# Performance work log

Hardware: AMD Instinct MI355X
Metric: run time of the kernel (lower is better)

The kernel has to match this reference:

```python
import jax, jax.numpy as jnp
import numpy as np
import math

N = 50_000       # points (CSR segments)
V = 500_000      # mapped views (ragged rows)
IN_MAIN, IN_MAP, IN_MOD = 64, 16, 128
NC, NC_QK = 32, 8
EPS = 1e-12


def setup_inputs() -> dict:
    key = jax.random.key(0)
    ks = jax.random.split(key, 18)
    def rn(k, shape, fan_in=None):
        s = (1.0 / math.sqrt(fan_in)) if fan_in else 1.0
        return jax.random.normal(k, shape, jnp.float32) * s
    x_main = rn(ks[0], (N, IN_MAIN))
    x_mod = rn(ks[1], (V, IN_MOD))
    x_map = rn(ks[2], (V, IN_MAP))
    # CSR pointers: monotone, csr[0]=0, csr[-1]=V (full row coverage)
    inner = jnp.sort(jax.random.randint(ks[3], (N - 1,), 0, V))
    csr_idx = jnp.concatenate([jnp.zeros(1, jnp.int32), inner.astype(jnp.int32),
                               jnp.full((1,), V, jnp.int32)])
    return {
        "x_main": x_main, "x_mod": x_mod, "x_map": x_map, "csr_idx": csr_idx,
        # E_main: MLP([in_main, nc, nc], bias=False)
        "W_main1": rn(ks[4], (IN_MAIN, NC), IN_MAIN),
        "W_main2": rn(ks[5], (NC, NC), NC),
        # E_map (DeepSetFeat): elementwise MLP + segment-max set context + fuse
        "W_map1": rn(ks[6], (IN_MAP, NC), IN_MAP),
        "W_map2": rn(ks[7], (2 * NC, NC), 2 * NC),
        # E_mod: MLP([in_mod, in_mod, in_mod], bias=False)
        "W_mod1": rn(ks[8], (IN_MOD, IN_MOD), IN_MOD),
        "W_mod2": rn(ks[9], (IN_MOD, IN_MOD), IN_MOD),
        # Q, K linear heads (nc_inner -> nc_qk * num_groups), with bias
        "WQ": rn(ks[10], (NC, NC_QK), NC), "bQ": jnp.zeros((NC_QK,), jnp.float32),
        "WK": rn(ks[11], (NC, NC_QK), NC), "bK": jnp.zeros((NC_QK,), jnp.float32),
        # Gating(num_groups=1): weight init ones, bias init zeros
        "g_w": jnp.ones((1, 1), jnp.float32), "g_b": jnp.zeros((1, 1), jnp.float32),
    }


def reference(x_main, x_mod, x_map, csr_idx,
              W_main1, W_main2, W_map1, W_map2, W_mod1, W_mod2,
              WQ, bQ, WK, bK, g_w, g_b):
    counts = csr_idx[1:] - csr_idx[:-1]                     # [N]
    dense_idx = jnp.repeat(jnp.arange(N, dtype=jnp.int32), counts,
                           total_repeat_length=V)           # [V]
    nonempty = counts > 0                                   # [N]

    # --- encoders ---
    h_main = jax.nn.relu(x_main @ W_main1) @ W_main2        # [N, NC]
    h = jax.nn.relu(x_map @ W_map1)                         # [V, NC]
    set_ctx = jax.ops.segment_max(h, dense_idx, num_segments=N)
    set_ctx = jnp.where(nonempty[:, None], set_ctx, 0.0)    # empty segs -> 0
    h_map = jax.nn.relu(jnp.concatenate([h, set_ctx[dense_idx]], axis=1) @ W_map2)  # [V, NC]
    h_mod = jax.nn.relu(x_mod @ W_mod1) @ W_mod2            # [V, IN_MOD]

    # --- Q/K compatibilities (num_groups=1) ---
    keys = h_map @ WK + bK                                  # [V, NC_QK]
    queries = (h_main @ WQ + bQ)[dense_idx]                 # [V, NC_QK]
    comp = jnp.sum(keys * queries, axis=1) / jnp.sqrt(jnp.float32(NC_QK))  # [V]

    # --- segment_softmax_csr ---
    seg_max = jax.ops.segment_max(comp, dense_idx, num_segments=N)
    seg_max = jnp.where(nonempty, seg_max, 0.0)
    cexp = jnp.exp(comp - seg_max[dense_idx])               # [V]
    seg_sum = jax.ops.segment_sum(cexp, dense_idx, num_segments=N) + EPS
    att = cexp / seg_sum[dense_idx]                         # [V]

    # --- attention-weighted pooling ---
    x_pool = jax.ops.segment_sum(h_mod * att[:, None], dense_idx, num_segments=N)  # [N, IN_MOD]

    # --- gating on per-segment max compatibility ---
    gate_in = jnp.where(nonempty, seg_max, 0.0)[:, None]    # [N, 1]
    gate = jnp.tanh(jax.nn.relu(g_w * gate_in + g_b))       # [N, 1]
    x_pool = x_pool * gate

    x_seen = nonempty
    return x_pool, x_seen
```

## Files before the change

### kernel.cpp

```cpp
#include <hip/hip_runtime.h>
#include <math.h>

#define N_PTS 50000
#define V_VIEWS 500000
#define IN_MAIN 64
#define IN_MAP 16
#define IN_MOD 128
#define NC 32
#define NC_QK 8
#define SEG_EPS 1e-12f

typedef short bf16x8 __attribute__((ext_vector_type(8)));
typedef float f32x4 __attribute__((ext_vector_type(4)));

static __device__ __forceinline__ short f2bf(float x) {
    union { float f; unsigned u; } v; v.f = x;
    unsigned r = v.u + 0x7fffu + ((v.u >> 16) & 1u);
    return (short)(r >> 16);
}


__global__ __launch_bounds__(256) void k0_setup(const int* __restrict__ csr,
                                                const float* __restrict__ Wmod1,
                                                const float* __restrict__ Wmod2,
                                                const float* __restrict__ Wm1,
                                                const float* __restrict__ Wm2,
                                                int* __restrict__ didx,
                                                float* __restrict__ pooled,
                                                float* __restrict__ ctxw,
                                                short* __restrict__ Wf,
                                                short* __restrict__ W1f,
                                                short* __restrict__ W2af,
                                                short* __restrict__ W2f) {
    int t = blockIdx.x * blockDim.x + threadIdx.x;
    int total = gridDim.x * blockDim.x;
    if (t < N_PTS) {
        int a = csr[t], b = csr[t + 1];
        for (int v = a; v < b; ++v) didx[v] = t;
    }
    for (int i = t; i < N_PTS * IN_MOD; i += total) pooled[i] = 0.f;
    for (int i = t; i < N_PTS * NC; i += total) ctxw[i] = 0.f;
    for (int i = t; i < IN_MOD * IN_MOD; i += total) {
        int e = i & 7, l = (i >> 3) & 63, j = (i >> 9) & 7, kk = i >> 12;
        int k = kk * 32 + ((l >> 4) << 3) + e;
        int ch = (j << 4) + (l & 15);
        Wf[i] = f2bf(Wmod1[k * IN_MOD + ch]);
        W2f[i] = f2bf(Wmod2[k * IN_MOD + ch]);
    }
    for (int i = t; i < 1024; i += total) {
        int e = i & 7, l = (i >> 3) & 63, j = i >> 9;
        int k = ((l >> 4) << 3) + e;
        int ch = (j << 4) + (l & 15);
        W1f[i] = (k < IN_MAP) ? f2bf(Wm1[k * NC + ch]) : (short)0;
        W2af[i] = f2bf(Wm2[k * NC + ch]);
    }
}

__global__ __launch_bounds__(256) void kA_main_q(
    const float* __restrict__ x_main, const float* __restrict__ W1,
    const float* __restrict__ W2, const float* __restrict__ WQ,
    const float* __restrict__ bQ, const float* __restrict__ WK,
    const float* __restrict__ bK,
    float* __restrict__ wq, float* __restrict__ qb) {
    __shared__ float W1l[IN_MAIN * NC];
    __shared__ float W2l[NC * NC];
    __shared__ float WQl[NC * NC_QK];
    __shared__ float WKl[NC * NC_QK];
    __shared__ float bQl[NC_QK];
    __shared__ float bKl[NC_QK];
    __shared__ float h1buf[8][NC];
    __shared__ float h2buf[8][NC];
    __shared__ float qbuf[8][NC_QK];
    int tid = threadIdx.x;
    for (int i = tid; i < IN_MAIN * NC; i += 256) W1l[i] = W1[i];
    for (int i = tid; i < NC * NC; i += 256) W2l[i] = W2[i];
    for (int i = tid; i < NC * NC_QK; i += 256) WQl[i] = WQ[i];
    for (int i = tid; i < NC * NC_QK; i += 256) WKl[i] = WK[i];
    if (tid < NC_QK) { bQl[tid] = bQ[tid]; bKl[tid] = bK[tid]; }
    __syncthreads();
    int g = tid >> 5, c = tid & 31;
    int p = blockIdx.x * 8 + g;
    float h1 = 0.f;
    if (p < N_PTS) {
        const float* xr = x_main + (size_t)p * IN_MAIN;
        for (int k = 0; k < IN_MAIN; ++k) h1 += xr[k] * W1l[k * NC + c];
        h1 = fmaxf(h1, 0.f);
    }
    h1buf[g][c] = h1;
    __syncthreads();
    float h2 = 0.f;
    for (int j = 0; j < NC; ++j) h2 += h1buf[g][j] * W2l[j * NC + c];
    h2buf[g][c] = h2;
    __syncthreads();
    if (c < NC_QK) {
        float acc = bQl[c];
        for (int j = 0; j < NC; ++j) acc += h2buf[g][j] * WQl[j * NC_QK + c];
        qbuf[g][c] = acc;
    }
    __syncthreads();
    if (p < N_PTS) {
        float w = 0.f;
        for (int j = 0; j < NC_QK; ++j) w += WKl[c * NC_QK + j] * qbuf[g][j];
        wq[(size_t)p * NC + c] = w;
        if (c == 0) {
            float b = 0.f;
            for (int j = 0; j < NC_QK; ++j) b += bKl[j] * qbuf[g][j];
            qb[p] = b;
        }
    }
}

__global__ __launch_bounds__(256) void kH_ctx(
    const float* __restrict__ x_map, const int* __restrict__ didx,
    const short* __restrict__ W1f, int* __restrict__ ctxbits) {
    int tid = threadIdx.x;
    int w = tid >> 6, lane = tid & 63;
    int vbase = blockIdx.x * 64 + w * 16;
    if (vbase >= V_VIEWS) return;
    const bf16x8* pW1 = (const bf16x8*)W1f;
    bf16x8 b1a = pW1[lane], b1b = pW1[64 + lane];

    bf16x8 a1 = (bf16x8){0, 0, 0, 0, 0, 0, 0, 0};
    if (lane < 32) {
        const float* xp = x_map + (size_t)(vbase + (lane & 15)) * IN_MAP + ((lane >> 4) << 3);
        float4 x0 = *(const float4*)xp;
        float4 x1 = *(const float4*)(xp + 4);
        a1[0] = f2bf(x0.x); a1[1] = f2bf(x0.y); a1[2] = f2bf(x0.z); a1[3] = f2bf(x0.w);
        a1[4] = f2bf(x1.x); a1[5] = f2bf(x1.y); a1[6] = f2bf(x1.z); a1[7] = f2bf(x1.w);
    }
    f32x4 d1a = (f32x4){0.f, 0.f, 0.f, 0.f}, d1b = (f32x4){0.f, 0.f, 0.f, 0.f};
    d1a = __builtin_amdgcn_mfma_f32_16x16x32_bf16(a1, b1a, d1a, 0, 0, 0);
    d1b = __builtin_amdgcn_mfma_f32_16x16x32_bf16(a1, b1b, d1b, 0, 0, 0);

    int c = lane & 15, kq = lane >> 4;
    int vg = vbase + (kq << 2);
    int4 ss = *(const int4*)(didx + vg);
    const int* sp = (const int*)&ss;
    float ma = 0.f, mb = 0.f;
#pragma unroll
    for (int r = 0; r < 4; ++r) {
        ma = fmaxf(ma, fmaxf(d1a[r], 0.f));
        mb = fmaxf(mb, fmaxf(d1b[r], 0.f));
        bool runend = (r == 3) || (sp[r + 1] != sp[r]);
        if (runend) {
            atomicMax(&ctxbits[sp[r] * NC + c], __float_as_int(ma));
            atomicMax(&ctxbits[sp[r] * NC + c + 16], __float_as_int(mb));
            ma = 0.f; mb = 0.f;
        }
    }
}

__global__ __launch_bounds__(256) void kB2b_ctxw(
    const float* __restrict__ Wm2, float* __restrict__ ctxw) {
    __shared__ float W2bl[NC * NC];
    __shared__ float ctxl[8][NC];
    int tid = threadIdx.x;
    for (int i = tid; i < NC * NC; i += 256) W2bl[i] = Wm2[NC * NC + i];
    int g = tid >> 5, c = tid & 31;
    int s = blockIdx.x * 8 + g;
    float cv = (s < N_PTS) ? ctxw[(size_t)s * NC + c] : 0.f;
    ctxl[g][c] = cv;
    __syncthreads();
    if (s < N_PTS) {
        float val = 0.f;
        for (int j = 0; j < NC; ++j) val += ctxl[g][j] * W2bl[j * NC + c];
        ctxw[(size_t)s * NC + c] = val;
    }
}

__global__ __launch_bounds__(256) void kB3_comp(
    const float* __restrict__ x_map, const int* __restrict__ didx,
    const short* __restrict__ W1f, const short* __restrict__ W2af,
    const float* __restrict__ ctxW2b, const float* __restrict__ wq,
    const float* __restrict__ qb, float* __restrict__ comp) {
    __shared__ float hl[4][16 * 36];
    int tid = threadIdx.x;
    int w = tid >> 6, lane = tid & 63;
    int vbase = blockIdx.x * 64 + w * 16;
    if (vbase >= V_VIEWS) return;
    const bf16x8* pW1 = (const bf16x8*)W1f;
    const bf16x8* pW2 = (const bf16x8*)W2af;
    bf16x8 b1a = pW1[lane], b1b = pW1[64 + lane];
    bf16x8 b2a = pW2[lane], b2b = pW2[64 + lane];

    bf16x8 a1 = (bf16x8){0, 0, 0, 0, 0, 0, 0, 0};
    if (lane < 32) {
        const float* xp = x_map + (size_t)(vbase + (lane & 15)) * IN_MAP + ((lane >> 4) << 3);
        float4 x0 = *(const float4*)xp;
        float4 x1 = *(const float4*)(xp + 4);
        a1[0] = f2bf(x0.x); a1[1] = f2bf(x0.y); a1[2] = f2bf(x0.z); a1[3] = f2bf(x0.w);
        a1[4] = f2bf(x1.x); a1[5] = f2bf(x1.y); a1[6] = f2bf(x1.z); a1[7] = f2bf(x1.w);
    }
    f32x4 d1a = (f32x4){0.f, 0.f, 0.f, 0.f}, d1b = (f32x4){0.f, 0.f, 0.f, 0.f};
    d1a = __builtin_amdgcn_mfma_f32_16x16x32_bf16(a1, b1a, d1a, 0, 0, 0);
    d1b = __builtin_amdgcn_mfma_f32_16x16x32_bf16(a1, b1b, d1b, 0, 0, 0);

    float* hw = hl[w];
    int c = lane & 15;
    int vr0 = (lane >> 4) << 2;
#pragma unroll
    for (int r = 0; r < 4; ++r) {
        hw[(vr0 + r) * 36 + c] = fmaxf(d1a[r], 0.f);
        hw[(vr0 + r) * 36 + c + 16] = fmaxf(d1b[r], 0.f);
    }
    const float* hr = hw + (lane & 15) * 36 + ((lane >> 4) << 3);
    float4 h0 = *(const float4*)hr;
    float4 h1 = *(const float4*)(hr + 4);
    bf16x8 a2;
    a2[0] = f2bf(h0.x); a2[1] = f2bf(h0.y); a2[2] = f2bf(h0.z); a2[3] = f2bf(h0.w);
    a2[4] = f2bf(h1.x); a2[5] = f2bf(h1.y); a2[6] = f2bf(h1.z); a2[7] = f2bf(h1.w);

    f32x4 d2a = (f32x4){0.f, 0.f, 0.f, 0.f}, d2b = (f32x4){0.f, 0.f, 0.f, 0.f};
    d2a = __builtin_amdgcn_mfma_f32_16x16x32_bf16(a2, b2a, d2a, 0, 0, 0);
    d2b = __builtin_amdgcn_mfma_f32_16x16x32_bf16(a2, b2b, d2b, 0, 0, 0);

    int vg = vbase + vr0;
    int4 ss = *(const int4*)(didx + vg);
    const int* sp = (const int*)&ss;
    float part[4];
#pragma unroll
    for (int r = 0; r < 4; ++r) {
        size_t so = (size_t)sp[r] * NC;
        float m0 = fmaxf(d2a[r] + ctxW2b[so + c], 0.f);
        float m1 = fmaxf(d2b[r] + ctxW2b[so + c + 16], 0.f);
        part[r] = m0 * wq[so + c] + m1 * wq[so + c + 16];
    }
#pragma unroll
    for (int mask = 1; mask < 16; mask <<= 1) {
#pragma unroll
        for (int r = 0; r < 4; ++r) part[r] += __shfl_xor(part[r], mask);
    }
    if (c == 0) {
        const float inv_sqrt = 0.35355339059327373f;
        float4 o;
        o.x = (part[0] + qb[sp[0]]) * inv_sqrt;
        o.y = (part[1] + qb[sp[1]]) * inv_sqrt;
        o.z = (part[2] + qb[sp[2]]) * inv_sqrt;
        o.w = (part[3] + qb[sp[3]]) * inv_sqrt;
        *(float4*)(comp + vg) = o;
    }
}

__global__ __launch_bounds__(256) void kB4_att(
    float* __restrict__ comp, const int* __restrict__ csr,
    float* __restrict__ segmax) {
    int wid = threadIdx.x >> 6, lane = threadIdx.x & 63;
    int seg = blockIdx.x * 4 + wid;
    if (seg >= N_PTS) return;
    int v0 = csr[seg], v1 = csr[seg + 1];
    if (v0 >= v1) {
        if (lane == 0) segmax[seg] = 0.f;
        return;
    }
    float mx = -__builtin_inff();
    for (int v = v0 + lane; v < v1; v += 64) mx = fmaxf(mx, comp[v]);
    for (int o = 32; o > 0; o >>= 1) mx = fmaxf(mx, __shfl_xor(mx, o));
    float sm = 0.f;
    for (int v = v0 + lane; v < v1; v += 64) sm += __expf(comp[v] - mx);
    for (int o = 32; o > 0; o >>= 1) sm += __shfl_xor(sm, o);
    float inv = 1.f / (sm + SEG_EPS);
    for (int v = v0 + lane; v < v1; v += 64) comp[v] = __expf(comp[v] - mx) * inv;
    if (lane == 0) segmax[seg] = mx;
}

#define VB 64
__global__ __launch_bounds__(256) void kC_pool(
    const float* __restrict__ x_mod, const short* __restrict__ Wf,
    const int* __restrict__ didx, const int* __restrict__ csr,
    const float* __restrict__ att, float* __restrict__ pooled) {
    __shared__ float Yl[VB * 132];
    __shared__ float attl[VB];
    __shared__ int didxl[VB];
    int tid = threadIdx.x;
    int vbase = blockIdx.x * VB;
    if (tid < VB) {
        int v = vbase + tid;
        if (v < V_VIEWS) {
            didxl[tid] = didx[v];
            attl[tid] = att[v];
        } else {
            didxl[tid] = didx[V_VIEWS - 1];
            attl[tid] = 0.f;
        }
    }
    __syncthreads();

    int w = tid >> 6, lane = tid & 63;
    int row16 = lane & 15;
    int kq = lane >> 4;
    int k0 = kq << 3;
    f32x4 acc[8];
    for (int j = 0; j < 8; ++j) acc[j] = (f32x4){0.f, 0.f, 0.f, 0.f};

    int v = vbase + w * 16 + row16;
    if (v >= V_VIEWS) v = V_VIEWS - 1;
    const float* xp = x_mod + (size_t)v * IN_MOD;

#pragma unroll
    for (int kk = 0; kk < 4; ++kk) {
        float4 x0 = *(const float4*)(xp + kk * 32 + k0);
        float4 x1 = *(const float4*)(xp + kk * 32 + k0 + 4);
        bf16x8 a;
        a[0] = f2bf(x0.x); a[1] = f2bf(x0.y); a[2] = f2bf(x0.z); a[3] = f2bf(x0.w);
        a[4] = f2bf(x1.x); a[5] = f2bf(x1.y); a[6] = f2bf(x1.z); a[7] = f2bf(x1.w);
        const bf16x8* wf = (const bf16x8*)(Wf + ((size_t)(kk * 8) * 64 + lane) * 8);
#pragma unroll
        for (int j = 0; j < 8; ++j) {
            bf16x8 b = wf[j * 64];
            acc[j] = __builtin_amdgcn_mfma_f32_16x16x32_bf16(a, b, acc[j], 0, 0, 0);
        }
    }
#pragma unroll
    for (int j = 0; j < 8; ++j) {
        int ch = j * 16 + row16;
        int rbase = w * 16 + (kq << 2);
#pragma unroll
        for (int r = 0; r < 4; ++r) {
            int rw = rbase + r;
            Yl[rw * 132 + ch] = fmaxf(acc[j][r], 0.f) * attl[rw];
        }
    }
    __syncthreads();
    if (tid < IN_MOD) {
        int c = tid;
        float s_acc = 0.f;
        int cur = didxl[0];
        for (int r = 0; r < VB; ++r) {
            int s = didxl[r];
            if (s != cur) {
                if (csr[cur] >= vbase && csr[cur + 1] <= vbase + VB)
                    pooled[(size_t)cur * IN_MOD + c] = s_acc;
                else
                    atomicAdd(&pooled[(size_t)cur * IN_MOD + c], s_acc);
                s_acc = 0.f; cur = s;
            }
            s_acc += Yl[r * 132 + c];
        }
        if (csr[cur] >= vbase && csr[cur + 1] <= vbase + VB)
            pooled[(size_t)cur * IN_MOD + c] = s_acc;
        else
            atomicAdd(&pooled[(size_t)cur * IN_MOD + c], s_acc);
    }
}

__global__ __launch_bounds__(256) void kD_final(
    const short* __restrict__ W2f,
    const float* __restrict__ segmax, const int* __restrict__ csr,
    const float* __restrict__ g_w, const float* __restrict__ g_b,
    float* __restrict__ out) {
    int tid = threadIdx.x;
    int w = tid >> 6, lane = tid & 63;
    int row16 = lane & 15;
    int kq = lane >> 4;
    int k0 = kq << 3;
    int rbase = blockIdx.x * 64 + w * 16;
    float gw = g_w[0], gb = g_b[0];

    int rr = rbase + row16;
    if (rr >= N_PTS) rr = N_PTS - 1;
    const float* xp = out + (size_t)rr * IN_MOD;

    f32x4 acc[8];
    for (int j = 0; j < 8; ++j) acc[j] = (f32x4){0.f, 0.f, 0.f, 0.f};
#pragma unroll
    for (int kk = 0; kk < 4; ++kk) {
        float4 x0 = *(const float4*)(xp + kk * 32 + k0);
        float4 x1 = *(const float4*)(xp + kk * 32 + k0 + 4);
        bf16x8 a;
        a[0] = f2bf(x0.x); a[1] = f2bf(x0.y); a[2] = f2bf(x0.z); a[3] = f2bf(x0.w);
        a[4] = f2bf(x1.x); a[5] = f2bf(x1.y); a[6] = f2bf(x1.z); a[7] = f2bf(x1.w);
        const bf16x8* wf = (const bf16x8*)(W2f + ((size_t)(kk * 8) * 64 + lane) * 8);
#pragma unroll
        for (int j = 0; j < 8; ++j) {
            bf16x8 b = wf[j * 64];
            acc[j] = __builtin_amdgcn_mfma_f32_16x16x32_bf16(a, b, acc[j], 0, 0, 0);
        }
    }
    float gate[4];
    int rowv[4];
#pragma unroll
    for (int r = 0; r < 4; ++r) {
        int ro = rbase + (kq << 2) + r;
        rowv[r] = ro;
        if (ro < N_PTS) {
            bool nz = csr[ro + 1] > csr[ro];
            float gin = nz ? segmax[ro] : 0.f;
            gate[r] = tanhf(fmaxf(gw * gin + gb, 0.f));
            if (row16 == 0) out[(size_t)N_PTS * IN_MOD + ro] = nz ? 1.f : 0.f;
        } else {
            gate[r] = 0.f;
        }
    }
#pragma unroll
    for (int j = 0; j < 8; ++j) {
        int ch = j * 16 + row16;
#pragma unroll
        for (int r = 0; r < 4; ++r) {
            if (rowv[r] < N_PTS)
                out[(size_t)rowv[r] * IN_MOD + ch] = acc[j][r] * gate[r];
        }
    }
}

extern "C" void kernel_launch(void* const* d_in, const int* in_sizes, int n_in,
                              void* d_out, int out_size, void* d_ws, size_t ws_size,
                              hipStream_t stream) {
    (void)in_sizes; (void)n_in; (void)out_size; (void)ws_size;
    const float* x_main = (const float*)d_in[0];
    const float* x_mod  = (const float*)d_in[1];
    const float* x_map  = (const float*)d_in[2];
    const int*   csr    = (const int*)d_in[3];
    const float* W_main1 = (const float*)d_in[4];
    const float* W_main2 = (const float*)d_in[5];
    const float* W_map1  = (const float*)d_in[6];
    const float* W_map2  = (const float*)d_in[7];
    const float* W_mod1  = (const float*)d_in[8];
    const float* W_mod2  = (const float*)d_in[9];
    const float* WQ = (const float*)d_in[10];
    const float* bQ = (const float*)d_in[11];
    const float* WK = (const float*)d_in[12];
    const float* bK = (const float*)d_in[13];
    const float* g_w = (const float*)d_in[14];
    const float* g_b = (const float*)d_in[15];
    float* out = (float*)d_out;

    char* ws = (char*)d_ws;
    int*   didx   = (int*)ws;
    float* wq     = (float*)(ws + 2000000);
    float* qb     = (float*)(ws + 8400000);
    float* ctxw   = (float*)(ws + 8600000);
    float* comp   = (float*)(ws + 15000000);
    float* segmax = (float*)(ws + 17000000);
    short* Wf     = (short*)(ws + 17200000);
    short* W1f    = (short*)(ws + 17240000);
    short* W2af   = (short*)(ws + 17244000);
    short* W2f    = (short*)(ws + 17248000);
    float* pooled = out;

    k0_setup<<<512, 256, 0, stream>>>(csr, W_mod1, W_mod2, W_map1, W_map2,
                                      didx, pooled, ctxw, Wf, W1f, W2af, W2f);
    kA_main_q<<<(N_PTS + 7) / 8, 256, 0, stream>>>(x_main, W_main1, W_main2, WQ, bQ,
                                                   WK, bK, wq, qb);
    kH_ctx<<<(V_VIEWS + 63) / 64, 256, 0, stream>>>(x_map, didx, W1f, (int*)ctxw);
    kB2b_ctxw<<<(N_PTS + 7) / 8, 256, 0, stream>>>(W_map2, ctxw);
    kB3_comp<<<(V_VIEWS + 63) / 64, 256, 0, stream>>>(x_map, didx, W1f, W2af,
                                                      ctxw, wq, qb, comp);
    kB4_att<<<(N_PTS + 3) / 4, 256, 0, stream>>>(comp, csr, segmax);
    kC_pool<<<(V_VIEWS + VB - 1) / VB, 256, 0, stream>>>(x_mod, Wf, didx, csr,
                                                         comp, pooled);
    kD_final<<<(N_PTS + 63) / 64, 256, 0, stream>>>(W2f, segmax, csr, g_w, g_b, out);
}
```

Measured before the change: 235.0 us.

## Cache bf16 map hidden layer, defer softmax normalization, split pooling scan

kH_ctx now writes the first-layer map activations as bf16 to a workspace buffer, so kB3_comp loads them instead of rereading x_map and recomputing the first MFMA. kB4_att no longer rewrites comp with normalized attention. It stores a per-segment inverse sum, and kC_pool computes exp(comp - max) * invsum on the fly. The pooling segment scan in kC_pool is split across 256 threads as two 32-row halves instead of 128 threads over 64 rows, which may raise atomic traffic at the half boundary. The cost is an extra 32 MB bf16 write and read for hbuf in exchange for less recompute and one fewer full pass over comp.

```diff
diff --git a/kernel.cpp b/kernel.cpp
--- a/kernel.cpp
+++ b/kernel.cpp
@@ -112,7 +112,9 @@
 
 __global__ __launch_bounds__(256) void kH_ctx(
     const float* __restrict__ x_map, const int* __restrict__ didx,
-    const short* __restrict__ W1f, int* __restrict__ ctxbits) {
+    const short* __restrict__ W1f, int* __restrict__ ctxbits,
+    short* __restrict__ hbuf) {
+    __shared__ float hl[4][16 * 36];
     int tid = threadIdx.x;
     int w = tid >> 6, lane = tid & 63;
     int vbase = blockIdx.x * 64 + w * 16;
@@ -133,7 +135,22 @@
     d1b = __builtin_amdgcn_mfma_f32_16x16x32_bf16(a1, b1b, d1b, 0, 0, 0);
 
     int c = lane & 15, kq = lane >> 4;
-    int vg = vbase + (kq << 2);
+    int vr0 = kq << 2;
+    float* hw = hl[w];
+#pragma unroll
+    for (int r = 0; r < 4; ++r) {
+        hw[(vr0 + r) * 36 + c] = fmaxf(d1a[r], 0.f);
+        hw[(vr0 + r) * 36 + c + 16] = fmaxf(d1b[r], 0.f);
+    }
+    const float* hr = hw + c * 36 + (kq << 3);
+    float4 h0 = *(const float4*)hr;
+    float4 h1 = *(const float4*)(hr + 4);
+    bf16x8 a2;
+    a2[0] = f2bf(h0.x); a2[1] = f2bf(h0.y); a2[2] = f2bf(h0.z); a2[3] = f2bf(h0.w);
+    a2[4] = f2bf(h1.x); a2[5] = f2bf(h1.y); a2[6] = f2bf(h1.z); a2[7] = f2bf(h1.w);
+    *(bf16x8*)(hbuf + (size_t)(vbase + c) * NC + (kq << 3)) = a2;
+
+    int vg = vbase + vr0;
     int4 ss = *(const int4*)(didx + vg);
     const int* sp = (const int*)&ss;
     float ma = 0.f, mb = 0.f;
@@ -169,51 +186,24 @@
 }
 
 __global__ __launch_bounds__(256) void kB3_comp(
-    const float* __restrict__ x_map, const int* __restrict__ didx,
-    const short* __restrict__ W1f, const short* __restrict__ W2af,
+    const short* __restrict__ hbuf, const int* __restrict__ didx,
+    const short* __restrict__ W2af,
     const float* __restrict__ ctxW2b, const float* __restrict__ wq,
     const float* __restrict__ qb, float* __restrict__ comp) {
-    __shared__ float hl[4][16 * 36];
     int tid = threadIdx.x;
     int w = tid >> 6, lane = tid & 63;
     int vbase = blockIdx.x * 64 + w * 16;
     if (vbase >= V_VIEWS) return;
-    const bf16x8* pW1 = (const bf16x8*)W1f;
     const bf16x8* pW2 = (const bf16x8*)W2af;
-    bf16x8 b1a = pW1[lane], b1b = pW1[64 + lane];
     bf16x8 b2a = pW2[lane], b2b = pW2[64 + lane];
-
-    bf16x8 a1 = (bf16x8){0, 0, 0, 0, 0, 0, 0, 0};
-    if (lane < 32) {
-        const float* xp = x_map + (size_t)(vbase + (lane & 15)) * IN_MAP + ((lane >> 4) << 3);
-        float4 x0 = *(const float4*)xp;
-        float4 x1 = *(const float4*)(xp + 4);
-        a1[0] = f2bf(x0.x); a1[1] = f2bf(x0.y); a1[2] = f2bf(x0.z); a1[3] = f2bf(x0.w);
-        a1[4] = f2bf(x1.x); a1[5] = f2bf(x1.y); a1[6] = f2bf(x1.z); a1[7] = f2bf(x1.w);
-    }
-    f32x4 d1a = (f32x4){0.f, 0.f, 0.f, 0.f}, d1b = (f32x4){0.f, 0.f, 0.f, 0.f};
-    d1a = __builtin_amdgcn_mfma_f32_16x16x32_bf16(a1, b1a, d1a, 0, 0, 0);
-    d1b = __builtin_amdgcn_mfma_f32_16x16x32_bf16(a1, b1b, d1b, 0, 0, 0);
-
-    float* hw = hl[w];
-    int c = lane & 15;
-    int vr0 = (lane >> 4) << 2;
-#pragma unroll
-    for (int r = 0; r < 4; ++r) {
-        hw[(vr0 + r) * 36 + c] = fmaxf(d1a[r], 0.f);
-        hw[(vr0 + r) * 36 + c + 16] = fmaxf(d1b[r], 0.f);
-    }
-    const float* hr = hw + (lane & 15) * 36 + ((lane >> 4) << 3);
-    float4 h0 = *(const float4*)hr;
-    float4 h1 = *(const float4*)(hr + 4);
-    bf16x8 a2;
-    a2[0] = f2bf(h0.x); a2[1] = f2bf(h0.y); a2[2] = f2bf(h0.z); a2[3] = f2bf(h0.w);
-    a2[4] = f2bf(h1.x); a2[5] = f2bf(h1.y); a2[6] = f2bf(h1.z); a2[7] = f2bf(h1.w);
-
+    int c = lane & 15, kq = lane >> 4;
+
+    bf16x8 a2 = *(const bf16x8*)(hbuf + (size_t)(vbase + c) * NC + (kq << 3));
     f32x4 d2a = (f32x4){0.f, 0.f, 0.f, 0.f}, d2b = (f32x4){0.f, 0.f, 0.f, 0.f};
     d2a = __builtin_amdgcn_mfma_f32_16x16x32_bf16(a2, b2a, d2a, 0, 0, 0);
     d2b = __builtin_amdgcn_mfma_f32_16x16x32_bf16(a2, b2b, d2b, 0, 0, 0);
 
+    int vr0 = kq << 2;
     int vg = vbase + vr0;
     int4 ss = *(const int4*)(didx + vg);
     const int* sp = (const int*)&ss;
@@ -242,14 +232,14 @@
 }
 
 __global__ __launch_bounds__(256) void kB4_att(
-    float* __restrict__ comp, const int* __restrict__ csr,
-    float* __restrict__ segmax) {
+    const float* __restrict__ comp, const int* __restrict__ csr,
+    float* __restrict__ segmax, float* __restrict__ invsum) {
     int wid = threadIdx.x >> 6, lane = threadIdx.x & 63;
     int seg = blockIdx.x * 4 + wid;
     if (seg >= N_PTS) return;
     int v0 = csr[seg], v1 = csr[seg + 1];
     if (v0 >= v1) {
-        if (lane == 0) segmax[seg] = 0.f;
+        if (lane == 0) { segmax[seg] = 0.f; invsum[seg] = 0.f; }
         return;
     }
     float mx = -__builtin_inff();
@@ -258,16 +248,15 @@
     float sm = 0.f;
     for (int v = v0 + lane; v < v1; v += 64) sm += __expf(comp[v] - mx);
     for (int o = 32; o > 0; o >>= 1) sm += __shfl_xor(sm, o);
-    float inv = 1.f / (sm + SEG_EPS);
-    for (int v = v0 + lane; v < v1; v += 64) comp[v] = __expf(comp[v] - mx) * inv;
-    if (lane == 0) segmax[seg] = mx;
+    if (lane == 0) { segmax[seg] = mx; invsum[seg] = 1.f / (sm + SEG_EPS); }
 }
 
 #define VB 64
 __global__ __launch_bounds__(256) void kC_pool(
     const float* __restrict__ x_mod, const short* __restrict__ Wf,
     const int* __restrict__ didx, const int* __restrict__ csr,
-    const float* __restrict__ att, float* __restrict__ pooled) {
+    const float* __restrict__ comp, const float* __restrict__ segmax,
+    const float* __restrict__ invsum, float* __restrict__ pooled) {
     __shared__ float Yl[VB * 132];
     __shared__ float attl[VB];
     __shared__ int didxl[VB];
@@ -276,8 +265,9 @@
     if (tid < VB) {
         int v = vbase + tid;
         if (v < V_VIEWS) {
-            didxl[tid] = didx[v];
-            attl[tid] = att[v];
+            int s = didx[v];
+            didxl[tid] = s;
+            attl[tid] = __expf(comp[v] - segmax[s]) * invsum[s];
         } else {
             didxl[tid] = didx[V_VIEWS - 1];
             attl[tid] = 0.f;
@@ -321,25 +311,27 @@
         }
     }
     __syncthreads();
-    if (tid < IN_MOD) {
-        int c = tid;
+    {
+        int halfid = tid >> 7, cc = tid & 127;
+        int r0 = halfid << 5;
+        int hb = vbase + r0;
         float s_acc = 0.f;
-        int cur = didxl[0];
-        for (int r = 0; r < VB; ++r) {
+        int cur = didxl[r0];
+        for (int r = r0; r < r0 + 32; ++r) {
             int s = didxl[r];
             if (s != cur) {
-                if (csr[cur] >= vbase && csr[cur + 1] <= vbase + VB)
-                    pooled[(size_t)cur * IN_MOD + c] = s_acc;
+                if (csr[cur] >= hb && csr[cur + 1] <= hb + 32)
+                    pooled[(size_t)cur * IN_MOD + cc] = s_acc;
                 else
-                    atomicAdd(&pooled[(size_t)cur * IN_MOD + c], s_acc);
+                    atomicAdd(&pooled[(size_t)cur * IN_MOD + cc], s_acc);
                 s_acc = 0.f; cur = s;
             }
-            s_acc += Yl[r * 132 + c];
-        }
-        if (csr[cur] >= vbase && csr[cur + 1] <= vbase + VB)
-            pooled[(size_t)cur * IN_MOD + c] = s_acc;
+            s_acc += Yl[r * 132 + cc];
+        }
+        if (csr[cur] >= hb && csr[cur + 1] <= hb + 32)
+            pooled[(size_t)cur * IN_MOD + cc] = s_acc;
         else
-            atomicAdd(&pooled[(size_t)cur * IN_MOD + c], s_acc);
+            atomicAdd(&pooled[(size_t)cur * IN_MOD + cc], s_acc);
     }
 }
 
@@ -435,18 +427,20 @@
     short* W1f    = (short*)(ws + 17240000);
     short* W2af   = (short*)(ws + 17244000);
     short* W2f    = (short*)(ws + 17248000);
+    float* invsum = (float*)(ws + 17300000);
+    short* hbuf   = (short*)(ws + 17500000);
     float* pooled = out;
 
     k0_setup<<<512, 256, 0, stream>>>(csr, W_mod1, W_mod2, W_map1, W_map2,
                                       didx, pooled, ctxw, Wf, W1f, W2af, W2f);
     kA_main_q<<<(N_PTS + 7) / 8, 256, 0, stream>>>(x_main, W_main1, W_main2, WQ, bQ,
                                                    WK, bK, wq, qb);
-    kH_ctx<<<(V_VIEWS + 63) / 64, 256, 0, stream>>>(x_map, didx, W1f, (int*)ctxw);
+    kH_ctx<<<(V_VIEWS + 63) / 64, 256, 0, stream>>>(x_map, didx, W1f, (int*)ctxw, hbuf);
     kB2b_ctxw<<<(N_PTS + 7) / 8, 256, 0, stream>>>(W_map2, ctxw);
-    kB3_comp<<<(V_VIEWS + 63) / 64, 256, 0, stream>>>(x_map, didx, W1f, W2af,
+    kB3_comp<<<(V_VIEWS + 63) / 64, 256, 0, stream>>>(hbuf, didx, W2af,
                                                       ctxw, wq, qb, comp);
-    kB4_att<<<(N_PTS + 3) / 4, 256, 0, stream>>>(comp, csr, segmax);
+    kB4_att<<<(N_PTS + 3) / 4, 256, 0, stream>>>(comp, csr, segmax, invsum);
     kC_pool<<<(V_VIEWS + VB - 1) / VB, 256, 0, stream>>>(x_mod, Wf, didx, csr,
-                                                         comp, pooled);
+                                                         comp, segmax, invsum, pooled);
     kD_final<<<(N_PTS + 63) / 64, 256, 0, stream>>>(W2f, segmax, csr, g_w, g_b, out);
 }
```

Result: no change. 235.4 us (+0.2%).
